# Kernel optimization log

Hardware: AMD Instinct MI355X
Metric: run time of the kernel (lower is better)

The kernel has to match this reference:

```python
import jax, jax.numpy as jnp
import numpy as np

N_NODES = 100000
N_EDGES = 1600000
HIDDEN = 128


def setup_inputs() -> dict:
    key = jax.random.key(0)
    k_x, k_w1, k_w2, k_v, k_i, k_o = jax.random.split(key, 6)
    x = jax.random.normal(k_x, (N_NODES, HIDDEN), dtype=jnp.float32)
    # gate1/gate2 are Linear(hidden,1,bias=False); store their weight rows as vectors
    w1 = jax.random.normal(k_w1, (HIDDEN,), dtype=jnp.float32) * 0.1
    w2 = jax.random.normal(k_w2, (HIDDEN,), dtype=jnp.float32) * 0.1
    adj_vals = jax.random.uniform(k_v, (N_EDGES,), dtype=jnp.float32)
    in_idx = jax.random.randint(k_i, (N_EDGES,), 0, N_NODES, dtype=jnp.int32)
    out_idx = jax.random.randint(k_o, (N_EDGES,), 0, N_NODES, dtype=jnp.int32)
    return {"x": x, "w1": w1, "w2": w2, "adj_vals": adj_vals,
            "in_idx": in_idx, "out_idx": out_idx}


def reference(x, w1, w2, adj_vals, in_idx, out_idx):
    # per-node gate scalars: x1 = gate1(x), x2 = gate2(x)  -> [N]
    x1 = x @ w1
    x2 = x @ w2
    # edge gate: tanh(x1[src] + x2[dst]) * adj_value  (dropout is identity in eval mode)
    m = jnp.tanh(x1[in_idx] + x2[out_idx]) * adj_vals  # [E]
    # sparse.mm(adj_alpha, x): out[i] = sum_{e: row(e)=i} m_e * x[col(e)]
    messages = m[:, None] * x[out_idx]                 # [E, d]
    result = jax.ops.segment_sum(messages, in_idx, num_segments=N_NODES)
    return result
```

## Files before the change

kernel.cpp:

```cpp
#include <hip/hip_runtime.h>

#define N_NODES 100000
#define N_EDGES 1600000
#define HIDDEN  128

#define NPB_SHIFT 9
#define NPB       512
#define NB        ((N_NODES + NPB - 1) / NPB)
#define PART_EPT  16
#define PART_EPB  (256 * PART_EPT)
#define PART_B    ((N_EDGES + PART_EPB - 1) / PART_EPB)
#define GATES_B   ((N_NODES * 32 + 255) / 256)
#define FINE_PE   20

#define SCAN_C 16
#define SCAN_T ((N_NODES + SCAN_C - 1) / SCAN_C)
#define SCAN_THREADS 6400
#define SCAN_B (SCAN_THREADS / 256)

__device__ __forceinline__ ushort f2bf(float f) {
    unsigned int u = __float_as_uint(f);
    u = (u + 0x7FFFu + ((u >> 16) & 1u)) >> 16;
    return (ushort)u;
}

__global__ void fagcn_gates_hist(const float* __restrict__ x,
                                 const float* __restrict__ w1,
                                 const float* __restrict__ w2,
                                 const int*   __restrict__ in_idx,
                                 float* __restrict__ g1,
                                 float* __restrict__ g2,
                                 int*   __restrict__ bcnt,
                                 ushort* __restrict__ xh,
                                 int write_xh,
                                 int with_hist) {
    __shared__ int cnt[NB];
    if ((int)blockIdx.x < GATES_B) {
        const int tid  = blockIdx.x * 256 + (int)threadIdx.x;
        const int node = tid >> 5;
        const int hl   = (int)(threadIdx.x & 31);
        if (node >= N_NODES) return;

        const float4 xv  = *reinterpret_cast<const float4*>(x  + (size_t)node * HIDDEN + hl * 4);
        const float4 w1v = *reinterpret_cast<const float4*>(w1 + hl * 4);
        const float4 w2v = *reinterpret_cast<const float4*>(w2 + hl * 4);

        if (write_xh) {
            ushort4 h;
            h.x = f2bf(xv.x); h.y = f2bf(xv.y); h.z = f2bf(xv.z); h.w = f2bf(xv.w);
            *reinterpret_cast<ushort4*>(xh + (size_t)node * HIDDEN + hl * 4) = h;
        }

        float s1 = xv.x * w1v.x + xv.y * w1v.y + xv.z * w1v.z + xv.w * w1v.w;
        float s2 = xv.x * w2v.x + xv.y * w2v.y + xv.z * w2v.z + xv.w * w2v.w;

        #pragma unroll
        for (int off = 16; off > 0; off >>= 1) {
            s1 += __shfl_down(s1, off, 32);
            s2 += __shfl_down(s2, off, 32);
        }
        if (hl == 0) { g1[node] = s1; g2[node] = s2; }
    } else if (with_hist) {
        const int tid  = (int)threadIdx.x;
        const int base = ((int)blockIdx.x - GATES_B) * PART_EPB + tid * PART_EPT;
        for (int j = tid; j < NB; j += 256) cnt[j] = 0;
        __syncthreads();
        if (base < N_EDGES) {
            #pragma unroll
            for (int i = 0; i < 4; ++i) {
                const int4 v = *reinterpret_cast<const int4*>(in_idx + base + i * 4);
                atomicAdd(&cnt[v.x >> NPB_SHIFT], 1);
                atomicAdd(&cnt[v.y >> NPB_SHIFT], 1);
                atomicAdd(&cnt[v.z >> NPB_SHIFT], 1);
                atomicAdd(&cnt[v.w >> NPB_SHIFT], 1);
            }
        }
        __syncthreads();
        for (int j = tid; j < NB; j += 256)
            if (cnt[j]) atomicAdd(&bcnt[j], cnt[j]);
    }
}

__global__ void fagcn_part(const float* __restrict__ adj,
                           const int*   __restrict__ in_idx,
                           const int*   __restrict__ out_idx,
                           const float* __restrict__ g1,
                           const float* __restrict__ g2,
                           const int*   __restrict__ bcnt,
                           int*         __restrict__ bcur,
                           int2*        __restrict__ stage) {
    __shared__ int scan[256];
    __shared__ int sbase[NB], cnt[NB], lbase[NB], lcur[NB];
    const int tid  = (int)threadIdx.x;
    const int base = blockIdx.x * PART_EPB + tid * PART_EPT;

    const int c0 = (tid < NB) ? bcnt[tid] : 0;
    scan[tid] = c0;
    __syncthreads();
    for (int off = 1; off < 256; off <<= 1) {
        int v = (tid >= off) ? scan[tid - off] : 0;
        __syncthreads();
        scan[tid] += v;
        __syncthreads();
    }
    if (tid < NB) sbase[tid] = scan[tid] - c0;
    for (int j = tid; j < NB; j += 256) { cnt[j] = 0; lcur[j] = 0; }
    __syncthreads();

    int s[PART_EPT];
    const bool act = (base < N_EDGES);
    if (act) {
        #pragma unroll
        for (int i = 0; i < 4; ++i) {
            const int4 v = *reinterpret_cast<const int4*>(in_idx + base + i * 4);
            s[4 * i + 0] = v.x; s[4 * i + 1] = v.y;
            s[4 * i + 2] = v.z; s[4 * i + 3] = v.w;
        }
        #pragma unroll
        for (int i = 0; i < PART_EPT; ++i)
            atomicAdd(&cnt[s[i] >> NPB_SHIFT], 1);
    }
    __syncthreads();
    for (int j = tid; j < NB; j += 256)
        if (cnt[j] > 0) lbase[j] = sbase[j] + atomicAdd(&bcur[j], cnt[j]);
    __syncthreads();
    if (act) {
        #pragma unroll
        for (int i = 0; i < 4; ++i) {
            const int4   d4 = *reinterpret_cast<const int4*>(out_idx + base + i * 4);
            const float4 a4 = *reinterpret_cast<const float4*>(adj + base + i * 4);
            const int   dd[4] = {d4.x, d4.y, d4.z, d4.w};
            const float aa[4] = {a4.x, a4.y, a4.z, a4.w};
            #pragma unroll
            for (int k = 0; k < 4; ++k) {
                const int src = s[4 * i + k];
                const int dst = dd[k];
                const float m = tanhf(g1[src] + g2[dst]) * aa[k];
                const int b   = src >> NPB_SHIFT;
                const int pos = lbase[b] + atomicAdd(&lcur[b], 1);
                stage[pos] = make_int2(((src & (NPB - 1)) << 17) | dst,
                                       __float_as_int(m));
            }
        }
    }
}

__global__ void fagcn_fine(const int2* __restrict__ stage,
                           const int*  __restrict__ bcnt,
                           int*        __restrict__ offsets,
                           int2*       __restrict__ sedge) {
    __shared__ int cnt[NPB];
    __shared__ int cur[NPB];
    __shared__ int s_ebeg;
    const int b = (int)blockIdx.x;
    const int t = (int)threadIdx.x;

    if (t < 64) {
        int s = 0;
        for (int j = t; j < b; j += 64) s += bcnt[j];
        #pragma unroll
        for (int off = 32; off > 0; off >>= 1) s += __shfl_down(s, off, 64);
        if (t == 0) s_ebeg = s;
    }
    cnt[t] = 0;
    __syncthreads();

    const int ebeg = s_ebeg;
    const int eend = ebeg + bcnt[b];

    int2 pay[FINE_PE];
    #pragma unroll
    for (int i = 0; i < FINE_PE; ++i) {
        const int e = ebeg + t + i * NPB;
        if (e < eend) {
            pay[i] = stage[e];
            atomicAdd(&cnt[pay[i].x >> 17], 1);
        }
    }
    __syncthreads();

    const int c = cnt[t];
    for (int off = 1; off < NPB; off <<= 1) {
        int v = (t >= off) ? cnt[t - off] : 0;
        __syncthreads();
        cnt[t] += v;
        __syncthreads();
    }
    const int excl = cnt[t] - c;
    cur[t] = ebeg + excl;
    const int node = (b << NPB_SHIFT) + t;
    if (node < N_NODES) offsets[node] = ebeg + excl;
    if (b == (int)gridDim.x - 1 && t == 0) offsets[N_NODES] = N_EDGES;
    __syncthreads();

    #pragma unroll
    for (int i = 0; i < FINE_PE; ++i) {
        const int e = ebeg + t + i * NPB;
        if (e < eend) {
            const int pos = atomicAdd(&cur[pay[i].x >> 17], 1);
            sedge[pos] = make_int2(pay[i].x & 0x1FFFF, pay[i].y);
        }
    }
}

__device__ __forceinline__ void acc8(float* a, uint4 v, float m) {
    const unsigned int u[4] = {v.x, v.y, v.z, v.w};
    #pragma unroll
    for (int i = 0; i < 4; ++i) {
        const float lo = __uint_as_float(u[i] << 16);
        const float hi = __uint_as_float(u[i] & 0xFFFF0000u);
        a[2 * i]     += m * lo;
        a[2 * i + 1] += m * hi;
    }
}

__global__ void fagcn_gather_bf16(const ushort* __restrict__ xh,
                                  const int*   __restrict__ offsets,
                                  const int2*  __restrict__ sedge,
                                  float*       __restrict__ out,
                                  int node_beg, int node_end) {
    const int wave = node_beg + (int)((blockIdx.x * blockDim.x + threadIdx.x) >> 6);
    const int lane = (int)(threadIdx.x & 63);
    if (wave >= node_end) return;

    const int beg = offsets[wave];
    const int end = offsets[wave + 1];
    const int q   = lane >> 4;
    const int ql  = lane & 15;

    float a[8] = {0.f, 0.f, 0.f, 0.f, 0.f, 0.f, 0.f, 0.f};
    float b[8] = {0.f, 0.f, 0.f, 0.f, 0.f, 0.f, 0.f, 0.f};

    int e = beg + q;
    for (; e + 12 < end; e += 16) {
        const int2 ed0 = sedge[e];
        const int2 ed1 = sedge[e + 4];
        const int2 ed2 = sedge[e + 8];
        const int2 ed3 = sedge[e + 12];
        const uint4 v0 = *reinterpret_cast<const uint4*>(xh + (size_t)ed0.x * HIDDEN + ql * 8);
        const uint4 v1 = *reinterpret_cast<const uint4*>(xh + (size_t)ed1.x * HIDDEN + ql * 8);
        const uint4 v2 = *reinterpret_cast<const uint4*>(xh + (size_t)ed2.x * HIDDEN + ql * 8);
        const uint4 v3 = *reinterpret_cast<const uint4*>(xh + (size_t)ed3.x * HIDDEN + ql * 8);
        acc8(a, v0, __int_as_float(ed0.y));
        acc8(b, v1, __int_as_float(ed1.y));
        acc8(a, v2, __int_as_float(ed2.y));
        acc8(b, v3, __int_as_float(ed3.y));
    }
    for (; e < end; e += 4) {
        const int2 ed = sedge[e];
        const uint4 v = *reinterpret_cast<const uint4*>(xh + (size_t)ed.x * HIDDEN + ql * 8);
        acc8(a, v, __int_as_float(ed.y));
    }

    float r[8];
    #pragma unroll
    for (int i = 0; i < 8; ++i) r[i] = a[i] + b[i];
    #pragma unroll
    for (int i = 0; i < 8; ++i) r[i] += __shfl(r[i], lane ^ 16, 64);
    #pragma unroll
    for (int i = 0; i < 8; ++i) r[i] += __shfl(r[i], lane ^ 32, 64);

    if (lane < 16) {
        float* o = out + (size_t)wave * HIDDEN + ql * 8;
        float4 lo = {r[0], r[1], r[2], r[3]};
        float4 hi = {r[4], r[5], r[6], r[7]};
        *reinterpret_cast<float4*>(o)     = lo;
        *reinterpret_cast<float4*>(o + 4) = hi;
    }
}

__global__ void fagcn_hist(const int* __restrict__ in_idx,
                           int* __restrict__ counts) {
    const int e = blockIdx.x * blockDim.x + threadIdx.x;
    if (e < N_EDGES) atomicAdd(&counts[in_idx[e]], 1);
}

__global__ void fagcn_scan1(const int* __restrict__ counts,
                            int* __restrict__ tsum) {
    const int t = blockIdx.x * blockDim.x + threadIdx.x;
    if (t >= SCAN_THREADS) return;
    int s = 0;
    if (t < SCAN_T) {
        const int beg = t * SCAN_C;
        const int end = (beg + SCAN_C < N_NODES) ? beg + SCAN_C : N_NODES;
        for (int i = beg; i < end; ++i) s += counts[i];
    }
    tsum[t] = s;
}

__global__ void fagcn_scan2(int* __restrict__ tsum) {
    __shared__ int lsum[1024];
    const int t = (int)threadIdx.x;
    const int C = (SCAN_THREADS + 1023) / 1024;
    const int beg = t * C;
    const int end = (beg + C < SCAN_THREADS) ? beg + C : SCAN_THREADS;
    int s = 0;
    for (int i = beg; i < end; ++i) s += tsum[i];
    lsum[t] = s;
    __syncthreads();
    for (int off = 1; off < 1024; off <<= 1) {
        int v = (t >= off) ? lsum[t - off] : 0;
        __syncthreads();
        lsum[t] += v;
        __syncthreads();
    }
    int prefix = (t == 0) ? 0 : lsum[t - 1];
    for (int i = beg; i < end; ++i) {
        const int v = tsum[i];
        tsum[i] = prefix;
        prefix += v;
    }
}

__global__ void fagcn_scan3(int* counts,
                            const int* __restrict__ tsum,
                            int* __restrict__ offsets) {
    const int t = blockIdx.x * blockDim.x + threadIdx.x;
    if (t >= SCAN_T) return;
    const int beg = t * SCAN_C;
    const int end = (beg + SCAN_C < N_NODES) ? beg + SCAN_C : N_NODES;
    int prefix = tsum[t];
    for (int i = beg; i < end; ++i) {
        const int c = counts[i];
        offsets[i] = prefix;
        prefix += c;
        counts[i] = 0;
    }
    if (t == 0) offsets[N_NODES] = N_EDGES;
}

__global__ void fagcn_bin(const float* __restrict__ adj,
                          const int*   __restrict__ in_idx,
                          const int*   __restrict__ out_idx,
                          const float* __restrict__ g1,
                          const float* __restrict__ g2,
                          const int*   __restrict__ offsets,
                          int*         __restrict__ cursor,
                          int2*        __restrict__ sedge) {
    const int e = blockIdx.x * blockDim.x + threadIdx.x;
    if (e >= N_EDGES) return;
    const int src = in_idx[e];
    const int dst = out_idx[e];
    const float m = tanhf(g1[src] + g2[dst]) * adj[e];
    const int pos = offsets[src] + atomicAdd(&cursor[src], 1);
    sedge[pos] = make_int2(dst, __float_as_int(m));
}

__global__ void fagcn_gather_f32(const float* __restrict__ x,
                                 const int*   __restrict__ offsets,
                                 const int2*  __restrict__ sedge,
                                 float*       __restrict__ out) {
    const int wave = (int)((blockIdx.x * blockDim.x + threadIdx.x) >> 6);
    const int lane = (int)(threadIdx.x & 63);
    if (wave >= N_NODES) return;
    const int beg  = offsets[wave];
    const int end  = offsets[wave + 1];
    const int half = lane >> 5;
    const int hl   = lane & 31;
    float4 a0 = {0.f, 0.f, 0.f, 0.f};
    float4 a1 = {0.f, 0.f, 0.f, 0.f};
    int e = beg + half;
    for (; e + 2 < end; e += 4) {
        const int2 ed0 = sedge[e];
        const int2 ed1 = sedge[e + 2];
        const float m0 = __int_as_float(ed0.y);
        const float m1 = __int_as_float(ed1.y);
        const float4 v0 = *reinterpret_cast<const float4*>(x + (size_t)ed0.x * HIDDEN + hl * 4);
        const float4 v1 = *reinterpret_cast<const float4*>(x + (size_t)ed1.x * HIDDEN + hl * 4);
        a0.x += m0 * v0.x; a0.y += m0 * v0.y; a0.z += m0 * v0.z; a0.w += m0 * v0.w;
        a1.x += m1 * v1.x; a1.y += m1 * v1.y; a1.z += m1 * v1.z; a1.w += m1 * v1.w;
    }
    for (; e < end; e += 2) {
        const int2 ed = sedge[e];
        const float m = __int_as_float(ed.y);
        const float4 v = *reinterpret_cast<const float4*>(x + (size_t)ed.x * HIDDEN + hl * 4);
        a0.x += m * v.x; a0.y += m * v.y; a0.z += m * v.z; a0.w += m * v.w;
    }
    float4 a;
    a.x = a0.x + a1.x; a.y = a0.y + a1.y; a.z = a0.z + a1.z; a.w = a0.w + a1.w;
    a.x += __shfl(a.x, lane ^ 32, 64);
    a.y += __shfl(a.y, lane ^ 32, 64);
    a.z += __shfl(a.z, lane ^ 32, 64);
    a.w += __shfl(a.w, lane ^ 32, 64);
    if (half == 0) {
        *reinterpret_cast<float4*>(out + (size_t)wave * HIDDEN + hl * 4) = a;
    }
}

extern "C" void kernel_launch(void* const* d_in, const int* in_sizes, int n_in,
                              void* d_out, int out_size, void* d_ws, size_t ws_size,
                              hipStream_t stream) {
    const float* x        = (const float*)d_in[0];
    const float* w1       = (const float*)d_in[1];
    const float* w2       = (const float*)d_in[2];
    const float* adj_vals = (const float*)d_in[3];
    const int*   in_idx   = (const int*)d_in[4];
    const int*   out_idx  = (const int*)d_in[5];
    float* out = (float*)d_out;

    ushort* xh      = (ushort*)d_ws;
    int2*   sedge   = (int2*)(xh + (size_t)N_NODES * HIDDEN);
    int2*   stage   = sedge + N_EDGES;
    float*  g1      = (float*)(stage + N_EDGES);
    float*  g2      = g1 + N_NODES;
    int*    offsets = (int*)(g2 + N_NODES);
    int*    cursor  = offsets + N_NODES + 1;
    int*    tsum    = cursor + N_NODES;
    int*    bcnt    = tsum + SCAN_THREADS;
    int*    bcur    = bcnt + NB;

    const size_t need_full = (size_t)((char*)(bcur + NB) - (char*)d_ws);
    const size_t need_old  = need_full - (size_t)N_EDGES * 8;
    const int full_path = (ws_size >= need_full);
    const int bf16_ok   = (ws_size >= need_old);

    if (full_path) {
        hipMemsetAsync(bcnt, 0, (size_t)(2 * NB) * sizeof(int), stream);
        fagcn_gates_hist<<<GATES_B + PART_B, 256, 0, stream>>>(
            x, w1, w2, in_idx, g1, g2, bcnt, xh, 1, 1);
        fagcn_part<<<PART_B, 256, 0, stream>>>(
            adj_vals, in_idx, out_idx, g1, g2, bcnt, bcur, stage);
        fagcn_fine<<<NB, NPB, 0, stream>>>(stage, bcnt, offsets, sedge);
        const int half_nodes = N_NODES / 2;
        fagcn_gather_bf16<<<(half_nodes + 3) / 4, 256, 0, stream>>>(
            xh, offsets, sedge, out, 0, half_nodes);
        fagcn_gather_bf16<<<(N_NODES - half_nodes + 3) / 4, 256, 0, stream>>>(
            xh, offsets, sedge, out, half_nodes, N_NODES);
    } else {
        if (!bf16_ok) sedge = (int2*)d_ws;
        fagcn_gates_hist<<<GATES_B, 256, 0, stream>>>(
            x, w1, w2, in_idx, g1, g2, bcnt, xh, bf16_ok, 0);
        hipMemsetAsync(cursor, 0, (size_t)N_NODES * sizeof(int), stream);
        fagcn_hist<<<(N_EDGES + 255) / 256, 256, 0, stream>>>(in_idx, cursor);
        fagcn_scan1<<<SCAN_B, 256, 0, stream>>>(cursor, tsum);
        fagcn_scan2<<<1, 1024, 0, stream>>>(tsum);
        fagcn_scan3<<<SCAN_B, 256, 0, stream>>>(cursor, tsum, offsets);
        fagcn_bin<<<(N_EDGES + 255) / 256, 256, 0, stream>>>(
            adj_vals, in_idx, out_idx, g1, g2, offsets, cursor, sedge);
        if (bf16_ok) {
            fagcn_gather_bf16<<<(N_NODES + 3) / 4, 256, 0, stream>>>(
                xh, offsets, sedge, out, 0, N_NODES);
        } else {
            fagcn_gather_f32<<<(N_NODES + 3) / 4, 256, 0, stream>>>(
                x, offsets, sedge, out);
        }
    }
}
```

Before: 162.6 us.

## Hoist bucket prefix scan into separate kernel and halve partition edges per thread

Moves the per-block redundant 196-bucket prefix scan out of every partition block and the per-block serial prefix sum in the fine-sort kernel into one small scan kernel that writes bucket bases and resets cursors. Partition blocks now process 8 edges per thread, doubling the grid for more parallelism, while the histogram keeps 16 per thread. The memset calls are replaced by tiny zeroing kernels. This adds two extra kernel launches, and the smaller partition blocks do more global atomics on bucket cursors.

```diff
diff --git a/kernel.cpp b/kernel.cpp
--- a/kernel.cpp
+++ b/kernel.cpp
@@ -7,9 +7,12 @@
 #define NPB_SHIFT 9
 #define NPB       512
 #define NB        ((N_NODES + NPB - 1) / NPB)
-#define PART_EPT  16
+#define PART_EPT  8
 #define PART_EPB  (256 * PART_EPT)
 #define PART_B    ((N_EDGES + PART_EPB - 1) / PART_EPB)
+#define HIST_EPT  16
+#define HIST_EPB  (256 * HIST_EPT)
+#define HIST_B    ((N_EDGES + HIST_EPB - 1) / HIST_EPB)
 #define GATES_B   ((N_NODES * 32 + 255) / 256)
 #define FINE_PE   20
 
@@ -22,6 +25,11 @@
     unsigned int u = __float_as_uint(f);
     u = (u + 0x7FFFu + ((u >> 16) & 1u)) >> 16;
     return (ushort)u;
+}
+
+__global__ void fagcn_zero(int* __restrict__ bcnt) {
+    const int t = (int)threadIdx.x;
+    if (t < NB) bcnt[t] = 0;
 }
 
 __global__ void fagcn_gates_hist(const float* __restrict__ x,
@@ -62,7 +70,7 @@
         if (hl == 0) { g1[node] = s1; g2[node] = s2; }
     } else if (with_hist) {
         const int tid  = (int)threadIdx.x;
-        const int base = ((int)blockIdx.x - GATES_B) * PART_EPB + tid * PART_EPT;
+        const int base = ((int)blockIdx.x - GATES_B) * HIST_EPB + tid * HIST_EPT;
         for (int j = tid; j < NB; j += 256) cnt[j] = 0;
         __syncthreads();
         if (base < N_EDGES) {
@@ -81,29 +89,36 @@
     }
 }
 
+__global__ void fagcn_scanb(const int* __restrict__ bcnt,
+                            int* __restrict__ sbase,
+                            int* __restrict__ bcur) {
+    __shared__ int l[256];
+    const int t = (int)threadIdx.x;
+    const int c = (t < NB) ? bcnt[t] : 0;
+    l[t] = c;
+    __syncthreads();
+    for (int off = 1; off < 256; off <<= 1) {
+        int v = (t >= off) ? l[t - off] : 0;
+        __syncthreads();
+        l[t] += v;
+        __syncthreads();
+    }
+    if (t < NB) { sbase[t] = l[t] - c; bcur[t] = 0; }
+    if (t == NB - 1) sbase[NB] = l[t];
+}
+
 __global__ void fagcn_part(const float* __restrict__ adj,
                            const int*   __restrict__ in_idx,
                            const int*   __restrict__ out_idx,
                            const float* __restrict__ g1,
                            const float* __restrict__ g2,
-                           const int*   __restrict__ bcnt,
+                           const int*   __restrict__ sbase,
                            int*         __restrict__ bcur,
                            int2*        __restrict__ stage) {
-    __shared__ int scan[256];
-    __shared__ int sbase[NB], cnt[NB], lbase[NB], lcur[NB];
+    __shared__ int cnt[NB], lbase[NB], lcur[NB];
     const int tid  = (int)threadIdx.x;
     const int base = blockIdx.x * PART_EPB + tid * PART_EPT;
 
-    const int c0 = (tid < NB) ? bcnt[tid] : 0;
-    scan[tid] = c0;
-    __syncthreads();
-    for (int off = 1; off < 256; off <<= 1) {
-        int v = (tid >= off) ? scan[tid - off] : 0;
-        __syncthreads();
-        scan[tid] += v;
-        __syncthreads();
-    }
-    if (tid < NB) sbase[tid] = scan[tid] - c0;
     for (int j = tid; j < NB; j += 256) { cnt[j] = 0; lcur[j] = 0; }
     __syncthreads();
 
@@ -111,7 +126,7 @@
     const bool act = (base < N_EDGES);
     if (act) {
         #pragma unroll
-        for (int i = 0; i < 4; ++i) {
+        for (int i = 0; i < PART_EPT / 4; ++i) {
             const int4 v = *reinterpret_cast<const int4*>(in_idx + base + i * 4);
             s[4 * i + 0] = v.x; s[4 * i + 1] = v.y;
             s[4 * i + 2] = v.z; s[4 * i + 3] = v.w;
@@ -126,7 +141,7 @@
     __syncthreads();
     if (act) {
         #pragma unroll
-        for (int i = 0; i < 4; ++i) {
+        for (int i = 0; i < PART_EPT / 4; ++i) {
             const int4   d4 = *reinterpret_cast<const int4*>(out_idx + base + i * 4);
             const float4 a4 = *reinterpret_cast<const float4*>(adj + base + i * 4);
             const int   dd[4] = {d4.x, d4.y, d4.z, d4.w};
@@ -146,27 +161,19 @@
 }
 
 __global__ void fagcn_fine(const int2* __restrict__ stage,
-                           const int*  __restrict__ bcnt,
+                           const int*  __restrict__ sbase,
                            int*        __restrict__ offsets,
                            int2*       __restrict__ sedge) {
     __shared__ int cnt[NPB];
     __shared__ int cur[NPB];
-    __shared__ int s_ebeg;
     const int b = (int)blockIdx.x;
     const int t = (int)threadIdx.x;
 
-    if (t < 64) {
-        int s = 0;
-        for (int j = t; j < b; j += 64) s += bcnt[j];
-        #pragma unroll
-        for (int off = 32; off > 0; off >>= 1) s += __shfl_down(s, off, 64);
-        if (t == 0) s_ebeg = s;
-    }
+    const int ebeg = sbase[b];
+    const int eend = sbase[b + 1];
+
     cnt[t] = 0;
     __syncthreads();
-
-    const int ebeg = s_ebeg;
-    const int eend = ebeg + bcnt[b];
 
     int2 pay[FINE_PE];
     #pragma unroll
@@ -273,6 +280,11 @@
                            int* __restrict__ counts) {
     const int e = blockIdx.x * blockDim.x + threadIdx.x;
     if (e < N_EDGES) atomicAdd(&counts[in_idx[e]], 1);
+}
+
+__global__ void fagcn_zero_nodes(int* __restrict__ counts) {
+    const int i = blockIdx.x * blockDim.x + threadIdx.x;
+    if (i < N_NODES) counts[i] = 0;
 }
 
 __global__ void fagcn_scan1(const int* __restrict__ counts,
@@ -407,7 +419,8 @@
     int*    cursor  = offsets + N_NODES + 1;
     int*    tsum    = cursor + N_NODES;
     int*    bcnt    = tsum + SCAN_THREADS;
-    int*    bcur    = bcnt + NB;
+    int*    sbase   = bcnt + NB;
+    int*    bcur    = sbase + NB + 1;
 
     const size_t need_full = (size_t)((char*)(bcur + NB) - (char*)d_ws);
     const size_t need_old  = need_full - (size_t)N_EDGES * 8;
@@ -415,12 +428,13 @@
     const int bf16_ok   = (ws_size >= need_old);
 
     if (full_path) {
-        hipMemsetAsync(bcnt, 0, (size_t)(2 * NB) * sizeof(int), stream);
-        fagcn_gates_hist<<<GATES_B + PART_B, 256, 0, stream>>>(
+        fagcn_zero<<<1, 256, 0, stream>>>(bcnt);
+        fagcn_gates_hist<<<GATES_B + HIST_B, 256, 0, stream>>>(
             x, w1, w2, in_idx, g1, g2, bcnt, xh, 1, 1);
+        fagcn_scanb<<<1, 256, 0, stream>>>(bcnt, sbase, bcur);
         fagcn_part<<<PART_B, 256, 0, stream>>>(
-            adj_vals, in_idx, out_idx, g1, g2, bcnt, bcur, stage);
-        fagcn_fine<<<NB, NPB, 0, stream>>>(stage, bcnt, offsets, sedge);
+            adj_vals, in_idx, out_idx, g1, g2, sbase, bcur, stage);
+        fagcn_fine<<<NB, NPB, 0, stream>>>(stage, sbase, offsets, sedge);
         const int half_nodes = N_NODES / 2;
         fagcn_gather_bf16<<<(half_nodes + 3) / 4, 256, 0, stream>>>(
             xh, offsets, sedge, out, 0, half_nodes);
@@ -430,7 +444,7 @@
         if (!bf16_ok) sedge = (int2*)d_ws;
         fagcn_gates_hist<<<GATES_B, 256, 0, stream>>>(
             x, w1, w2, in_idx, g1, g2, bcnt, xh, bf16_ok, 0);
-        hipMemsetAsync(cursor, 0, (size_t)N_NODES * sizeof(int), stream);
+        fagcn_zero_nodes<<<(N_NODES + 255) / 256, 256, 0, stream>>>(cursor);
         fagcn_hist<<<(N_EDGES + 255) / 256, 256, 0, stream>>>(in_idx, cursor);
         fagcn_scan1<<<SCAN_B, 256, 0, stream>>>(cursor, tsum);
         fagcn_scan2<<<1, 1024, 0, stream>>>(tsum);
```

Result: slower. 193.5 us (+19.0%).
